# Kernel optimization log

Measured on AMD Instinct MI355X. Metric: run time of the kernel, lower is better.

Reference implementation:

```python
import jax, jax.numpy as jnp
from jax import lax
import numpy as np

K = 2        # k-hop MIS / number of rw SpGEMM iterations
EPS = 0.5    # lazy random-walk epsilon
N = 2048     # nodes
D = 512      # feature dim
E = 65536    # edges (avg degree 32)


def setup_inputs() -> dict:
    key = jax.random.key(0)
    k1, k2, k3, k4 = jax.random.split(key, 4)
    edge_index = jax.random.randint(k1, (2, E), 0, N, dtype=jnp.int32)
    edge_attr = jax.random.uniform(k2, (E,), dtype=jnp.float32)
    x = jax.random.normal(k3, (N, D), dtype=jnp.float32)
    rank = jnp.arange(N, dtype=jnp.int32)  # node ordering ('random' ordering = some permutation; identity here)
    u = jax.random.uniform(k4, (N, N), dtype=jnp.float32)  # noise for row-wise multinomial sampling
    return {"edge_index": edge_index, "edge_attr": edge_attr, "x": x, "rank": rank, "u": u}


def _maximal_k_independent_set(row, col, rank, n, k):
    """Greedy maximal k-independent set: nodes that are local rank-minima within k hops."""
    big = jnp.int32(n)

    def prop_min(r):  # one hop of min-propagation (message row -> col), keep self
        return jnp.minimum(jax.ops.segment_min(r[row], col, num_segments=n), r)

    def prop_or(b):   # one hop of boolean OR propagation (as int32)
        return jnp.maximum(jax.ops.segment_max(b[row], col, num_segments=n), b)

    def cond(st):
        mis, mask, mr = st
        return ~jnp.all(mask)

    def body(st):
        mis, mask, mr = st
        for _ in range(k):
            mr = prop_min(mr)
        mis = mis | (rank == mr)
        mk = mis.astype(jnp.int32)
        for _ in range(k):
            mk = prop_or(mk)
        mask = mk > 0
        mr = jnp.where(mask, big, rank)
        return mis, mask, mr

    init = (jnp.zeros(n, bool), jnp.zeros(n, bool), rank)
    mis, _, _ = lax.while_loop(cond, body, init)
    return mis


def _row_normalize(m):
    s = m.sum(axis=1, keepdims=True)
    return m / jnp.where(s > 0, s, 1.0)


def reference(edge_index, edge_attr, x, rank, u):
    n = x.shape[0]
    row, col = edge_index[0], edge_index[1]

    # --- MIS over the graph structure (integer-only) ---
    mis = _maximal_k_independent_set(row, col, rank, n, K)

    # --- adjacency (dense padded form of the SparseTensor) ---
    adj = jnp.zeros((n, n), x.dtype).at[row, col].add(edge_attr)

    # --- lazy random walk: rw = D^-1 A, offdiag *= (1-eps), diag = old_diag + eps ---
    rw = _row_normalize(adj)
    di = jnp.arange(n)
    new_diag = rw[di, di] + EPS  # computed BEFORE scaling, per original code
    rw = (rw * (1.0 - EPS)).at[di, di].set(new_diag)

    # --- c_mat = rw^K @ eye[:, mis]; padded to [n, n] with zero non-MIS columns ---
    c = jnp.where(mis[None, :], jnp.eye(n, dtype=x.dtype), 0.0)
    for _ in range(K):
        c = rw @ c
    c = _row_normalize(c)

    # --- sample_partition_matrix: per-row multinomial via Gumbel-argmax ---
    g = -jnp.log(-jnp.log(u + 1e-20) + 1e-20)
    logits = jnp.where(c > 0, jnp.log(jnp.maximum(c, 1e-30)), -jnp.inf) + g
    cluster = jnp.argmax(logits, axis=1)                 # [n] cluster id (a MIS column)
    c_hard = jax.nn.one_hot(cluster, n, dtype=x.dtype)   # partition matrix [n, n]

    # --- p_inv = row-normalized c_hard.T ---
    counts = c_hard.sum(axis=0)
    p_inv = c_hard.T / jnp.where(counts > 0, counts, 1.0)[:, None]

    # --- coarsen: c^T A c, pool: p_inv @ x ---
    adj_c = c_hard.T @ adj @ c_hard
    x_pool = p_inv @ x
    return adj_c, c_hard, p_inv, mis, x_pool
```

## Files before the change

### kernel.cpp

```cpp
#include <hip/hip_runtime.h>
#include <hip/hip_bf16.h>
#include <math.h>
#include <stdint.h>

#define NN 2048
#define DD 512
#define EE 65536
#define EPSV 0.5f
#define SEN 2048
#define PADE 98304
#define CTILE 8

static const size_t SZ = (size_t)NN * NN;

__global__ __launch_bounds__(256) void count_deg(const int* __restrict__ row,
                                                 const int* __restrict__ col,
                                                 int* __restrict__ degree,
                                                 int* __restrict__ cdeg) {
  int e = blockIdx.x * 256 + threadIdx.x;
  atomicAdd(&degree[row[e]], 1);
  atomicAdd(&cdeg[col[e]], 1);
}

__global__ __launch_bounds__(1024) void csr_scan_pad(const int* __restrict__ degree,
                                                     const int* __restrict__ cdeg,
                                                     int* __restrict__ row_ptr,
                                                     int* __restrict__ fill_ptr,
                                                     int* __restrict__ col_ptr,
                                                     int* __restrict__ cfill_ptr,
                                                     unsigned short* __restrict__ colidx,
                                                     unsigned short* __restrict__ rowidx,
                                                     float* __restrict__ avals,
                                                     int* __restrict__ counts) {
  __shared__ int a[NN], b[NN], c[NN], d[NN];
  int t = threadIdx.x;
  for (int v = t; v < NN; v += 1024) {
    a[v] = (degree[v] + 15) & ~15;
    c[v] = (cdeg[v] + 15) & ~15;
    counts[v] = 0;
  }
  __syncthreads();
  int* s1 = a; int* d1 = b; int* s2 = c; int* d2 = d;
  for (int off = 1; off < NN; off <<= 1) {
    for (int v = t; v < NN; v += 1024) {
      d1[v] = s1[v] + (v >= off ? s1[v - off] : 0);
      d2[v] = s2[v] + (v >= off ? s2[v - off] : 0);
    }
    __syncthreads();
    int* tp = s1; s1 = d1; d1 = tp;
    tp = s2; s2 = d2; d2 = tp;
  }
  for (int v = t; v < NN; v += 1024) {
    int dg = degree[v];
    int end = s1[v];
    int excl = end - ((dg + 15) & ~15);
    row_ptr[v] = excl;
    fill_ptr[v] = excl;
    for (int e = excl + dg; e < end; ++e) {
      colidx[e] = (unsigned short)v;
      avals[e] = 0.f;
    }
    dg = cdeg[v];
    end = s2[v];
    excl = end - ((dg + 15) & ~15);
    col_ptr[v] = excl;
    cfill_ptr[v] = excl;
    for (int e = excl + dg; e < end; ++e) rowidx[e] = (unsigned short)v;
  }
  if (t == 0) {
    row_ptr[NN] = s1[NN - 1];
    col_ptr[NN] = s2[NN - 1];
  }
}

__global__ __launch_bounds__(256) void csr_fill(const int* __restrict__ row,
                                                const int* __restrict__ col,
                                                const float* __restrict__ attr,
                                                int* __restrict__ fill_ptr,
                                                int* __restrict__ cfill_ptr,
                                                unsigned short* __restrict__ colidx,
                                                unsigned short* __restrict__ rowidx,
                                                float* __restrict__ avals) {
  int e = blockIdx.x * 256 + threadIdx.x;
  int r = row[e], c = col[e];
  int pos = atomicAdd(&fill_ptr[r], 1);
  colidx[pos] = (unsigned short)c;
  avals[pos] = attr[e];
  rowidx[atomicAdd(&cfill_ptr[c], 1)] = (unsigned short)r;
}

__global__ __launch_bounds__(1024) void fused_mis_rw(const int* __restrict__ row_ptr_g,
                                                     const int* __restrict__ col_ptr_g,
                                                     const unsigned short* __restrict__ colidx,
                                                     const unsigned short* __restrict__ rowidx,
                                                     const int* __restrict__ rank_g,
                                                     int* __restrict__ mis_flag,
                                                     int* __restrict__ mis_list,
                                                     int* __restrict__ misinv,
                                                     int* __restrict__ mis_count,
                                                     const float* __restrict__ avals,
                                                     float* __restrict__ rw,
                                                     float* __restrict__ adjc,
                                                     float* __restrict__ xp) {
  if (blockIdx.x == 0) {
    __shared__ int rank_s[NN];
    __shared__ int mr[NN];
    __shared__ int cov[NN];
    __shared__ int dly[NN];
    __shared__ int mis_s[NN];
    __shared__ int row_ptr_s[NN + 1];
    __shared__ int col_ptr_s[NN + 1];
    __shared__ int unc[2][NN];
    __shared__ int dl[NN];
    __shared__ int ucnt[2];
    __shared__ int dcnt;
    __shared__ int cnt;
    int t = threadIdx.x;
    const uint4* col4 = (const uint4*)colidx;
    const uint4* row4 = (const uint4*)rowidx;

    for (int v = t; v < NN; v += 1024) {
      int rk = rank_g[v];
      rank_s[v] = rk;
      mr[v] = rk;
      cov[v] = 0;
      dly[v] = 0;
      mis_s[v] = 0;
      row_ptr_s[v] = row_ptr_g[v];
      col_ptr_s[v] = col_ptr_g[v];
      unc[0][v] = v;
    }
    if (t == 0) {
      row_ptr_s[NN] = row_ptr_g[NN];
      col_ptr_s[NN] = col_ptr_g[NN];
      ucnt[0] = NN;
      ucnt[1] = 0;
      dcnt = 0;
      cnt = 0;
    }
    __syncthreads();

    int cur = 0;
    for (int round = 0; round < NN; ++round) {
      int U = ucnt[cur];
      if (round) {
        for (int v = t; v < NN; v += 1024) {
          mr[v] = cov[v] ? SEN : rank_s[v];
          dly[v] = 0;
        }
        if (t == 0) { ucnt[cur ^ 1] = 0; dcnt = 0; }
        __syncthreads();
      }
      for (int i = t; i < U; i += 1024) {
        int v = unc[cur][i];
        int val = rank_s[v];
        int e0 = row_ptr_s[v];
        int nch = (row_ptr_s[v + 1] - e0) >> 3;
        const uint4* b4 = col4 + (e0 >> 3);
        for (int cI = 0; cI < nch; cI += 2) {
          uint4 A = b4[cI], B = b4[cI + 1];
          atomicMin(&mr[A.x & 0xFFFFu], val); atomicMin(&mr[A.x >> 16], val);
          atomicMin(&mr[A.y & 0xFFFFu], val); atomicMin(&mr[A.y >> 16], val);
          atomicMin(&mr[A.z & 0xFFFFu], val); atomicMin(&mr[A.z >> 16], val);
          atomicMin(&mr[A.w & 0xFFFFu], val); atomicMin(&mr[A.w >> 16], val);
          atomicMin(&mr[B.x & 0xFFFFu], val); atomicMin(&mr[B.x >> 16], val);
          atomicMin(&mr[B.y & 0xFFFFu], val); atomicMin(&mr[B.y >> 16], val);
          atomicMin(&mr[B.z & 0xFFFFu], val); atomicMin(&mr[B.z >> 16], val);
          atomicMin(&mr[B.w & 0xFFFFu], val); atomicMin(&mr[B.w >> 16], val);
        }
      }
      __syncthreads();
      for (int i = t; i < U; i += 1024) {
        int v = unc[cur][i];
        int val = mr[v];
        int e0 = col_ptr_s[v];
        int nch = (col_ptr_s[v + 1] - e0) >> 3;
        const uint4* b4 = row4 + (e0 >> 3);
        for (int cI = 0; cI < nch; cI += 2) {
          uint4 A = b4[cI], B = b4[cI + 1];
          int m0 = min(mr[A.x & 0xFFFFu], mr[A.x >> 16]);
          int m1 = min(mr[A.y & 0xFFFFu], mr[A.y >> 16]);
          int m2 = min(mr[A.z & 0xFFFFu], mr[A.z >> 16]);
          int m3 = min(mr[A.w & 0xFFFFu], mr[A.w >> 16]);
          int m4 = min(mr[B.x & 0xFFFFu], mr[B.x >> 16]);
          int m5 = min(mr[B.y & 0xFFFFu], mr[B.y >> 16]);
          int m6 = min(mr[B.z & 0xFFFFu], mr[B.z >> 16]);
          int m7 = min(mr[B.w & 0xFFFFu], mr[B.w >> 16]);
          val = min(val, min(min(min(m0, m1), min(m2, m3)),
                             min(min(m4, m5), min(m6, m7))));
        }
        if (rank_s[v] == val) {
          mis_s[v] = 1;
          dly[v] = 1;
          dl[atomicAdd(&dcnt, 1)] = v;
        }
      }
      __syncthreads();
      int D = dcnt;
      for (int i = t; i < D; i += 1024) {
        int v = dl[i];
        int e0 = row_ptr_s[v];
        int nch = (row_ptr_s[v + 1] - e0) >> 3;
        const uint4* b4 = col4 + (e0 >> 3);
        for (int cI = 0; cI < nch; cI += 2) {
          uint4 A = b4[cI], B = b4[cI + 1];
          dly[A.x & 0xFFFFu] = 1; dly[A.x >> 16] = 1;
          dly[A.y & 0xFFFFu] = 1; dly[A.y >> 16] = 1;
          dly[A.z & 0xFFFFu] = 1; dly[A.z >> 16] = 1;
          dly[A.w & 0xFFFFu] = 1; dly[A.w >> 16] = 1;
          dly[B.x & 0xFFFFu] = 1; dly[B.x >> 16] = 1;
          dly[B.y & 0xFFFFu] = 1; dly[B.y >> 16] = 1;
          dly[B.z & 0xFFFFu] = 1; dly[B.z >> 16] = 1;
          dly[B.w & 0xFFFFu] = 1; dly[B.w >> 16] = 1;
        }
      }
      __syncthreads();
      for (int i = t; i < U; i += 1024) {
        int v = unc[cur][i];
        int c1 = dly[v];
        if (!c1) {
          int e0 = col_ptr_s[v];
          int nch = (col_ptr_s[v + 1] - e0) >> 3;
          const uint4* b4 = row4 + (e0 >> 3);
          for (int cI = 0; cI < nch; cI += 2) {
            uint4 A = b4[cI], B = b4[cI + 1];
            c1 |= dly[A.x & 0xFFFFu] | dly[A.x >> 16] |
                  dly[A.y & 0xFFFFu] | dly[A.y >> 16] |
                  dly[A.z & 0xFFFFu] | dly[A.z >> 16] |
                  dly[A.w & 0xFFFFu] | dly[A.w >> 16] |
                  dly[B.x & 0xFFFFu] | dly[B.x >> 16] |
                  dly[B.y & 0xFFFFu] | dly[B.y >> 16] |
                  dly[B.z & 0xFFFFu] | dly[B.z >> 16] |
                  dly[B.w & 0xFFFFu] | dly[B.w >> 16];
            if (c1) break;
          }
        }
        if (c1) cov[v] = 1;
        else unc[cur ^ 1][atomicAdd(&ucnt[cur ^ 1], 1)] = v;
      }
      __syncthreads();
      if (ucnt[cur ^ 1] == 0) break;
      cur ^= 1;
    }

    for (int v = t; v < NN; v += 1024) {
      int s = mis_s[v];
      mis_flag[v] = s;
      int slot = -1;
      if (s) {
        slot = atomicAdd(&cnt, 1);
        mis_list[slot] = v;
      }
      misinv[v] = slot;
    }
    __syncthreads();
    if (t == 0) *mis_count = cnt;
  } else {
    __shared__ float rowbuf[NN];
    __shared__ float ssum;
    int i = blockIdx.x - 1;
    int t = threadIdx.x;
    float4 z4 = make_float4(0.f, 0.f, 0.f, 0.f);
    if (t < 512) ((float4*)(adjc + (size_t)i * NN))[t] = z4;
    if (t < 128) ((float4*)xp)[(size_t)i * 128 + t] = z4;
    for (int j = t; j < NN; j += 1024) rowbuf[j] = 0.f;
    if (t == 0) ssum = 0.f;
    __syncthreads();
    int e0 = row_ptr_g[i], e1 = row_ptr_g[i + 1];
    float part = 0.f;
    for (int e = e0 + t; e < e1; e += 1024) {
      float a = avals[e];
      atomicAdd(&rowbuf[colidx[e]], a);
      part += a;
    }
    for (int off = 32; off; off >>= 1) part += __shfl_down(part, off);
    if ((t & 63) == 0) atomicAdd(&ssum, part);
    __syncthreads();
    float s = ssum;
    s = (s > 0.f) ? s : 1.f;
    for (int j = t; j < NN; j += 1024) {
      float v = rowbuf[j] / s;
      v = (i == j) ? (v + EPSV) : (v * (1.f - EPSV));
      rw[(size_t)i * NN + j] = v;
    }
  }
}

__device__ inline unsigned int f32_key(float x) {
  unsigned int u = __float_as_uint(x);
  return (u & 0x80000000u) ? ~u : (u | 0x80000000u);
}
__device__ inline float dot4(float4 a, float4 b) {
  return ((a.x * b.x + a.y * b.y) + (a.z * b.z + a.w * b.w));
}
__device__ inline unsigned long long umax64(unsigned long long a, unsigned long long b) {
  return a > b ? a : b;
}
__device__ inline int pdecode(unsigned long long p) {
  return (p == 0ull) ? 0 : (NN - 1 - (int)(p & 0xFFFFFFFFull));
}

__global__ __launch_bounds__(256) void c2_cluster(const float* __restrict__ rw,
                                                  const float* __restrict__ u,
                                                  const int* __restrict__ mis_list,
                                                  const int* __restrict__ mis_count,
                                                  int* __restrict__ cluster,
                                                  int* __restrict__ counts) {
  __shared__ float Bs[CTILE][NN];
  int M = *mis_count;
  int t = threadIdx.x;
  int lane = t & 63, w = t >> 6;
  int r0 = blockIdx.x * 8 + w * 2;
  const float4* rp0 = (const float4*)(rw + (size_t)r0 * NN);
  const float4* rp1 = (const float4*)(rw + (size_t)(r0 + 1) * NN);
  float4 A0[8], A1[8];
#pragma unroll
  for (int q = 0; q < 8; ++q) {
    A0[q] = rp0[q * 64 + lane];
    A1[q] = rp1[q * 64 + lane];
  }
  unsigned long long best0 = 0ull, best1 = 0ull;
  for (int c0 = 0; c0 < M; c0 += CTILE) {
    int c1 = min(CTILE, M - c0);
    __syncthreads();
    for (int idx = t; idx < c1 * NN; idx += 256) {
      int c = idx >> 11, i = idx & (NN - 1);
      Bs[c][i] = rw[(size_t)i * NN + mis_list[c0 + c]];
    }
    __syncthreads();
    for (int jj = 0; jj < c1; ++jj) {
      int m = mis_list[c0 + jj];
      const float4* bb = (const float4*)(Bs[jj]);
      float4 B[8];
#pragma unroll
      for (int q = 0; q < 8; ++q) B[q] = bb[q * 64 + lane];
      float s01 = dot4(A0[0], B[0]) + dot4(A0[1], B[1]);
      float s23 = dot4(A0[2], B[2]) + dot4(A0[3], B[3]);
      float s45 = dot4(A0[4], B[4]) + dot4(A0[5], B[5]);
      float s67 = dot4(A0[6], B[6]) + dot4(A0[7], B[7]);
      float s = (s01 + s23) + (s45 + s67);
      s += __shfl_xor(s, 32);
      s += __shfl_xor(s, 16);
      s += __shfl_xor(s, 8);
      s += __shfl_xor(s, 4);
      s += __shfl_xor(s, 2);
      s += __shfl_xor(s, 1);
      float t01 = dot4(A1[0], B[0]) + dot4(A1[1], B[1]);
      float t23 = dot4(A1[2], B[2]) + dot4(A1[3], B[3]);
      float t45 = dot4(A1[4], B[4]) + dot4(A1[5], B[5]);
      float t67 = dot4(A1[6], B[6]) + dot4(A1[7], B[7]);
      float tt = (t01 + t23) + (t45 + t67);
      tt += __shfl_xor(tt, 32);
      tt += __shfl_xor(tt, 16);
      tt += __shfl_xor(tt, 8);
      tt += __shfl_xor(tt, 4);
      tt += __shfl_xor(tt, 2);
      tt += __shfl_xor(tt, 1);
      if (lane == 0) {
        if (s > 0.f) {
          float uu = u[(size_t)r0 * NN + m];
          float g = -logf(-logf(uu + 1e-20f) + 1e-20f);
          float logit = logf(s) + g;
          best0 = umax64(best0, ((unsigned long long)f32_key(logit) << 32) |
                                    (unsigned int)(NN - 1 - m));
        }
        if (tt > 0.f) {
          float uu = u[(size_t)(r0 + 1) * NN + m];
          float g = -logf(-logf(uu + 1e-20f) + 1e-20f);
          float logit = logf(tt) + g;
          best1 = umax64(best1, ((unsigned long long)f32_key(logit) << 32) |
                                    (unsigned int)(NN - 1 - m));
        }
      }
    }
  }
  if (lane == 0) {
    int m0b = pdecode(best0);
    cluster[r0] = m0b;
    atomicAdd(&counts[m0b], 1);
    int m1b = pdecode(best1);
    cluster[r0 + 1] = m1b;
    atomicAdd(&counts[m1b], 1);
  }
}

__global__ __launch_bounds__(256) void scatter_chpm(const int* __restrict__ row,
                                                    const int* __restrict__ col,
                                                    const float* __restrict__ attr,
                                                    const float* __restrict__ x,
                                                    const int* __restrict__ cluster,
                                                    const int* __restrict__ counts,
                                                    const int* __restrict__ mis_flag,
                                                    float* __restrict__ out_ch,
                                                    float* __restrict__ out_pinv,
                                                    float* __restrict__ out_mis,
                                                    float* __restrict__ adjc,
                                                    float* __restrict__ xp) {
  int idx = blockIdx.x * 256 + threadIdx.x;
  int a = idx >> 11, b = idx & (NN - 1);
  out_ch[idx] = (cluster[a] == b) ? 1.f : 0.f;
  float pv = 0.f;
  if (cluster[b] == a) {
    int c = counts[a];
    pv = 1.f / (float)(c > 0 ? c : 1);
  }
  out_pinv[idx] = pv;
  if (idx < NN) out_mis[idx] = mis_flag[idx] ? 1.f : 0.f;
  if (idx < NN * DD) {
    int i = idx >> 9;
    int ci = cluster[i];
    int c = counts[ci];
    atomicAdd(&xp[ci * DD + (idx & (DD - 1))], x[idx] / (float)(c > 0 ? c : 1));
  }
  if (idx < EE) {
    atomicAdd(&adjc[(size_t)cluster[row[idx]] * NN + cluster[col[idx]]], attr[idx]);
  }
}

extern "C" void kernel_launch(void* const* d_in, const int* in_sizes, int n_in,
                              void* d_out, int out_size, void* d_ws, size_t ws_size,
                              hipStream_t stream) {
  const int*   edge_index = (const int*)d_in[0];
  const float* edge_attr  = (const float*)d_in[1];
  const float* x          = (const float*)d_in[2];
  const int*   rank       = (const int*)d_in[3];
  const float* u          = (const float*)d_in[4];
  float* out              = (float*)d_out;

  const int* row = edge_index;
  const int* col = edge_index + EE;

  float* out_adjc = out;
  float* out_ch   = out + SZ;
  float* out_pinv = out + 2 * SZ;
  float* out_mis  = out + 3 * SZ;
  float* out_xp   = out + 3 * SZ + NN;

  int*   degree    = (int*)d_ws;
  int*   cdeg      = degree + NN;
  int*   counts    = cdeg + NN;
  int*   mis_flag  = counts + NN;
  int*   cluster   = mis_flag + NN;
  int*   mis_list  = cluster + NN;
  int*   misinv    = mis_list + NN;
  int*   mis_count = misinv + NN;
  int*   fill_ptr  = mis_count + 1;
  int*   cfill_ptr = fill_ptr + NN;
  int*   row_ptr   = cfill_ptr + NN;
  int*   col_ptr   = row_ptr + NN + 1;
  unsigned short* colidx =
      (unsigned short*)(((uintptr_t)(col_ptr + NN + 1) + 31) & ~(uintptr_t)31);
  unsigned short* rowidx = colidx + PADE;
  float* avals = (float*)(rowidx + PADE);

  hipMemsetAsync(d_ws, 0, 2 * NN * sizeof(int), stream);
  count_deg<<<EE / 256, 256, 0, stream>>>(row, col, degree, cdeg);
  csr_scan_pad<<<1, 1024, 0, stream>>>(degree, cdeg, row_ptr, fill_ptr, col_ptr,
                                       cfill_ptr, colidx, rowidx, avals, counts);
  csr_fill<<<EE / 256, 256, 0, stream>>>(row, col, edge_attr, fill_ptr, cfill_ptr,
                                         colidx, rowidx, avals);
  fused_mis_rw<<<NN + 1, 1024, 0, stream>>>(row_ptr, col_ptr, colidx, rowidx, rank,
                                            mis_flag, mis_list, misinv, mis_count,
                                            avals, out_pinv , out_adjc, out_xp);
  c2_cluster<<<256, 256, 0, stream>>>(out_pinv, u, mis_list, mis_count, cluster, counts);
  scatter_chpm<<<(NN * NN) / 256, 256, 0, stream>>>(row, col, edge_attr, x, cluster,
                                                    counts, mis_flag, out_ch, out_pinv,
                                                    out_mis, out_adjc, out_xp);
}
```

Baseline: 262.9 us.

## Merge CSR build into one kernel and pre-gather MIS columns once

The three CSR construction launches plus the memset become a single two-block kernel. Block 0 builds the row-major CSR and block 1 the column-major CSR, each counting degrees in shared memory. The cluster kernel no longer has every block re-gather the strided MIS columns of rw into shared memory. A separate gather kernel writes them once, contiguously, into the c_hard output buffer as scratch, and every block then streams them from global/L2 without barriers. Cluster decoding and counts move into a small extra kernel. This cuts redundant strided gathers and syncs, at the cost of serialising CSR building onto two blocks and reading B from L2 instead of LDS.

```diff
diff --git a/kernel.cpp b/kernel.cpp
--- a/kernel.cpp
+++ b/kernel.cpp
@@ -9,84 +9,79 @@
 #define EPSV 0.5f
 #define SEN 2048
 #define PADE 98304
-#define CTILE 8
 
 static const size_t SZ = (size_t)NN * NN;
 
-__global__ __launch_bounds__(256) void count_deg(const int* __restrict__ row,
-                                                 const int* __restrict__ col,
-                                                 int* __restrict__ degree,
-                                                 int* __restrict__ cdeg) {
-  int e = blockIdx.x * 256 + threadIdx.x;
-  atomicAdd(&degree[row[e]], 1);
-  atomicAdd(&cdeg[col[e]], 1);
-}
-
-__global__ __launch_bounds__(1024) void csr_scan_pad(const int* __restrict__ degree,
-                                                     const int* __restrict__ cdeg,
-                                                     int* __restrict__ row_ptr,
-                                                     int* __restrict__ fill_ptr,
-                                                     int* __restrict__ col_ptr,
-                                                     int* __restrict__ cfill_ptr,
-                                                     unsigned short* __restrict__ colidx,
-                                                     unsigned short* __restrict__ rowidx,
-                                                     float* __restrict__ avals,
-                                                     int* __restrict__ counts) {
-  __shared__ int a[NN], b[NN], c[NN], d[NN];
+__global__ __launch_bounds__(1024) void csr_build(const int* __restrict__ row,
+                                                  const int* __restrict__ col,
+                                                  const float* __restrict__ attr,
+                                                  int* __restrict__ row_ptr,
+                                                  int* __restrict__ col_ptr,
+                                                  unsigned short* __restrict__ colidx,
+                                                  unsigned short* __restrict__ rowidx,
+                                                  float* __restrict__ avals,
+                                                  unsigned long long* __restrict__ packed,
+                                                  int* __restrict__ counts) {
+  __shared__ int deg[NN];
+  __shared__ int sA[NN], sB[NN];
+  __shared__ int fptr[NN];
   int t = threadIdx.x;
+  int isCSR = (blockIdx.x == 0);
+  const int* key = isCSR ? row : col;
+  for (int v = t; v < NN; v += 1024) deg[v] = 0;
+  if (isCSR) {
+    for (int v = t; v < NN; v += 1024) {
+      packed[v] = 0ull;
+      counts[v] = 0;
+    }
+  }
+  __syncthreads();
+  for (int e = t; e < EE; e += 1024) atomicAdd(&deg[key[e]], 1);
+  __syncthreads();
+  for (int v = t; v < NN; v += 1024) sA[v] = (deg[v] + 15) & ~15;
+  __syncthreads();
+  int* s = sA;
+  int* d = sB;
+  for (int off = 1; off < NN; off <<= 1) {
+    for (int v = t; v < NN; v += 1024) d[v] = s[v] + (v >= off ? s[v - off] : 0);
+    __syncthreads();
+    int* tp = s; s = d; d = tp;
+  }
   for (int v = t; v < NN; v += 1024) {
-    a[v] = (degree[v] + 15) & ~15;
-    c[v] = (cdeg[v] + 15) & ~15;
-    counts[v] = 0;
+    int dg = deg[v];
+    int end = s[v];
+    int excl = end - ((dg + 15) & ~15);
+    fptr[v] = excl;
+    if (isCSR) {
+      row_ptr[v] = excl;
+      for (int e = excl + dg; e < end; ++e) {
+        colidx[e] = (unsigned short)v;
+        avals[e] = 0.f;
+      }
+    } else {
+      col_ptr[v] = excl;
+      for (int e = excl + dg; e < end; ++e) rowidx[e] = (unsigned short)v;
+    }
+  }
+  if (t == 0) {
+    if (isCSR) row_ptr[NN] = s[NN - 1];
+    else col_ptr[NN] = s[NN - 1];
   }
   __syncthreads();
-  int* s1 = a; int* d1 = b; int* s2 = c; int* d2 = d;
-  for (int off = 1; off < NN; off <<= 1) {
-    for (int v = t; v < NN; v += 1024) {
-      d1[v] = s1[v] + (v >= off ? s1[v - off] : 0);
-      d2[v] = s2[v] + (v >= off ? s2[v - off] : 0);
-    }
-    __syncthreads();
-    int* tp = s1; s1 = d1; d1 = tp;
-    tp = s2; s2 = d2; d2 = tp;
-  }
-  for (int v = t; v < NN; v += 1024) {
-    int dg = degree[v];
-    int end = s1[v];
-    int excl = end - ((dg + 15) & ~15);
-    row_ptr[v] = excl;
-    fill_ptr[v] = excl;
-    for (int e = excl + dg; e < end; ++e) {
-      colidx[e] = (unsigned short)v;
-      avals[e] = 0.f;
-    }
-    dg = cdeg[v];
-    end = s2[v];
-    excl = end - ((dg + 15) & ~15);
-    col_ptr[v] = excl;
-    cfill_ptr[v] = excl;
-    for (int e = excl + dg; e < end; ++e) rowidx[e] = (unsigned short)v;
-  }
-  if (t == 0) {
-    row_ptr[NN] = s1[NN - 1];
-    col_ptr[NN] = s2[NN - 1];
-  }
-}
-
-__global__ __launch_bounds__(256) void csr_fill(const int* __restrict__ row,
-                                                const int* __restrict__ col,
-                                                const float* __restrict__ attr,
-                                                int* __restrict__ fill_ptr,
-                                                int* __restrict__ cfill_ptr,
-                                                unsigned short* __restrict__ colidx,
-                                                unsigned short* __restrict__ rowidx,
-                                                float* __restrict__ avals) {
-  int e = blockIdx.x * 256 + threadIdx.x;
-  int r = row[e], c = col[e];
-  int pos = atomicAdd(&fill_ptr[r], 1);
-  colidx[pos] = (unsigned short)c;
-  avals[pos] = attr[e];
-  rowidx[atomicAdd(&cfill_ptr[c], 1)] = (unsigned short)r;
+  if (isCSR) {
+    for (int e = t; e < EE; e += 1024) {
+      int r = row[e];
+      int pos = atomicAdd(&fptr[r], 1);
+      colidx[pos] = (unsigned short)col[e];
+      avals[pos] = attr[e];
+    }
+  } else {
+    for (int e = t; e < EE; e += 1024) {
+      int c = col[e];
+      int pos = atomicAdd(&fptr[c], 1);
+      rowidx[pos] = (unsigned short)row[e];
+    }
+  }
 }
 
 __global__ __launch_bounds__(1024) void fused_mis_rw(const int* __restrict__ row_ptr_g,
@@ -286,6 +281,19 @@
   }
 }
 
+__global__ __launch_bounds__(256) void bc_gather(const float* __restrict__ rw,
+                                                 const int* __restrict__ mis_list,
+                                                 const int* __restrict__ mis_count,
+                                                 float* __restrict__ Bc) {
+  int M = *mis_count;
+  int total = M * NN;
+  int stride = gridDim.x * 256;
+  for (int j = blockIdx.x * 256 + threadIdx.x; j < total; j += stride) {
+    int tc = j >> 11, i = j & (NN - 1);
+    Bc[(size_t)tc * NN + i] = rw[(size_t)i * NN + mis_list[tc]];
+  }
+}
+
 __device__ inline unsigned int f32_key(float x) {
   unsigned int u = __float_as_uint(x);
   return (u & 0x80000000u) ? ~u : (u | 0x80000000u);
@@ -300,16 +308,14 @@
   return (p == 0ull) ? 0 : (NN - 1 - (int)(p & 0xFFFFFFFFull));
 }
 
-__global__ __launch_bounds__(256) void c2_cluster(const float* __restrict__ rw,
-                                                  const float* __restrict__ u,
-                                                  const int* __restrict__ mis_list,
-                                                  const int* __restrict__ mis_count,
-                                                  int* __restrict__ cluster,
-                                                  int* __restrict__ counts) {
-  __shared__ float Bs[CTILE][NN];
+__global__ __launch_bounds__(256) void c2_all(const float* __restrict__ rw,
+                                              const float* __restrict__ Bc,
+                                              const float* __restrict__ u,
+                                              const int* __restrict__ mis_list,
+                                              const int* __restrict__ mis_count,
+                                              unsigned long long* __restrict__ packed) {
   int M = *mis_count;
-  int t = threadIdx.x;
-  int lane = t & 63, w = t >> 6;
+  int lane = threadIdx.x & 63, w = threadIdx.x >> 6;
   int r0 = blockIdx.x * 8 + w * 2;
   const float4* rp0 = (const float4*)(rw + (size_t)r0 * NN);
   const float4* rp1 = (const float4*)(rw + (size_t)(r0 + 1) * NN);
@@ -320,68 +326,64 @@
     A1[q] = rp1[q * 64 + lane];
   }
   unsigned long long best0 = 0ull, best1 = 0ull;
-  for (int c0 = 0; c0 < M; c0 += CTILE) {
-    int c1 = min(CTILE, M - c0);
-    __syncthreads();
-    for (int idx = t; idx < c1 * NN; idx += 256) {
-      int c = idx >> 11, i = idx & (NN - 1);
-      Bs[c][i] = rw[(size_t)i * NN + mis_list[c0 + c]];
-    }
-    __syncthreads();
-    for (int jj = 0; jj < c1; ++jj) {
-      int m = mis_list[c0 + jj];
-      const float4* bb = (const float4*)(Bs[jj]);
-      float4 B[8];
+  for (int j = 0; j < M; ++j) {
+    int m = mis_list[j];
+    const float4* cb = (const float4*)(Bc + (size_t)j * NN);
+    float4 B[8];
 #pragma unroll
-      for (int q = 0; q < 8; ++q) B[q] = bb[q * 64 + lane];
-      float s01 = dot4(A0[0], B[0]) + dot4(A0[1], B[1]);
-      float s23 = dot4(A0[2], B[2]) + dot4(A0[3], B[3]);
-      float s45 = dot4(A0[4], B[4]) + dot4(A0[5], B[5]);
-      float s67 = dot4(A0[6], B[6]) + dot4(A0[7], B[7]);
-      float s = (s01 + s23) + (s45 + s67);
-      s += __shfl_xor(s, 32);
-      s += __shfl_xor(s, 16);
-      s += __shfl_xor(s, 8);
-      s += __shfl_xor(s, 4);
-      s += __shfl_xor(s, 2);
-      s += __shfl_xor(s, 1);
-      float t01 = dot4(A1[0], B[0]) + dot4(A1[1], B[1]);
-      float t23 = dot4(A1[2], B[2]) + dot4(A1[3], B[3]);
-      float t45 = dot4(A1[4], B[4]) + dot4(A1[5], B[5]);
-      float t67 = dot4(A1[6], B[6]) + dot4(A1[7], B[7]);
-      float tt = (t01 + t23) + (t45 + t67);
-      tt += __shfl_xor(tt, 32);
-      tt += __shfl_xor(tt, 16);
-      tt += __shfl_xor(tt, 8);
-      tt += __shfl_xor(tt, 4);
-      tt += __shfl_xor(tt, 2);
-      tt += __shfl_xor(tt, 1);
-      if (lane == 0) {
-        if (s > 0.f) {
-          float uu = u[(size_t)r0 * NN + m];
-          float g = -logf(-logf(uu + 1e-20f) + 1e-20f);
-          float logit = logf(s) + g;
-          best0 = umax64(best0, ((unsigned long long)f32_key(logit) << 32) |
-                                    (unsigned int)(NN - 1 - m));
-        }
-        if (tt > 0.f) {
-          float uu = u[(size_t)(r0 + 1) * NN + m];
-          float g = -logf(-logf(uu + 1e-20f) + 1e-20f);
-          float logit = logf(tt) + g;
-          best1 = umax64(best1, ((unsigned long long)f32_key(logit) << 32) |
-                                    (unsigned int)(NN - 1 - m));
-        }
+    for (int q = 0; q < 8; ++q) B[q] = cb[q * 64 + lane];
+    float s01 = dot4(A0[0], B[0]) + dot4(A0[1], B[1]);
+    float s23 = dot4(A0[2], B[2]) + dot4(A0[3], B[3]);
+    float s45 = dot4(A0[4], B[4]) + dot4(A0[5], B[5]);
+    float s67 = dot4(A0[6], B[6]) + dot4(A0[7], B[7]);
+    float s = (s01 + s23) + (s45 + s67);
+    s += __shfl_xor(s, 32);
+    s += __shfl_xor(s, 16);
+    s += __shfl_xor(s, 8);
+    s += __shfl_xor(s, 4);
+    s += __shfl_xor(s, 2);
+    s += __shfl_xor(s, 1);
+    float t01 = dot4(A1[0], B[0]) + dot4(A1[1], B[1]);
+    float t23 = dot4(A1[2], B[2]) + dot4(A1[3], B[3]);
+    float t45 = dot4(A1[4], B[4]) + dot4(A1[5], B[5]);
+    float t67 = dot4(A1[6], B[6]) + dot4(A1[7], B[7]);
+    float tt = (t01 + t23) + (t45 + t67);
+    tt += __shfl_xor(tt, 32);
+    tt += __shfl_xor(tt, 16);
+    tt += __shfl_xor(tt, 8);
+    tt += __shfl_xor(tt, 4);
+    tt += __shfl_xor(tt, 2);
+    tt += __shfl_xor(tt, 1);
+    if (lane == 0) {
+      if (s > 0.f) {
+        float uu = u[(size_t)r0 * NN + m];
+        float g = -logf(-logf(uu + 1e-20f) + 1e-20f);
+        float logit = logf(s) + g;
+        best0 = umax64(best0, ((unsigned long long)f32_key(logit) << 32) |
+                                  (unsigned int)(NN - 1 - m));
+      }
+      if (tt > 0.f) {
+        float uu = u[(size_t)(r0 + 1) * NN + m];
+        float g = -logf(-logf(uu + 1e-20f) + 1e-20f);
+        float logit = logf(tt) + g;
+        best1 = umax64(best1, ((unsigned long long)f32_key(logit) << 32) |
+                                  (unsigned int)(NN - 1 - m));
       }
     }
   }
   if (lane == 0) {
-    int m0b = pdecode(best0);
-    cluster[r0] = m0b;
-    atomicAdd(&counts[m0b], 1);
-    int m1b = pdecode(best1);
-    cluster[r0 + 1] = m1b;
-    atomicAdd(&counts[m1b], 1);
-  }
+    packed[r0] = best0;
+    packed[r0 + 1] = best1;
+  }
+}
+
+__global__ __launch_bounds__(256) void decode_cnt(const unsigned long long* __restrict__ packed,
+                                                  int* __restrict__ cluster,
+                                                  int* __restrict__ counts) {
+  int idx = blockIdx.x * 256 + threadIdx.x;
+  int m = pdecode(packed[idx]);
+  cluster[idx] = m;
+  atomicAdd(&counts[m], 1);
 }
 
 __global__ __launch_bounds__(256) void scatter_chpm(const int* __restrict__ row,
@@ -436,33 +438,28 @@
   float* out_mis  = out + 3 * SZ;
   float* out_xp   = out + 3 * SZ + NN;
 
-  int*   degree    = (int*)d_ws;
-  int*   cdeg      = degree + NN;
-  int*   counts    = cdeg + NN;
+  unsigned long long* packed = (unsigned long long*)d_ws;
+  int*   counts    = (int*)(packed + NN);
   int*   mis_flag  = counts + NN;
   int*   cluster   = mis_flag + NN;
   int*   mis_list  = cluster + NN;
   int*   misinv    = mis_list + NN;
   int*   mis_count = misinv + NN;
-  int*   fill_ptr  = mis_count + 1;
-  int*   cfill_ptr = fill_ptr + NN;
-  int*   row_ptr   = cfill_ptr + NN;
+  int*   row_ptr   = mis_count + 1;
   int*   col_ptr   = row_ptr + NN + 1;
   unsigned short* colidx =
       (unsigned short*)(((uintptr_t)(col_ptr + NN + 1) + 31) & ~(uintptr_t)31);
   unsigned short* rowidx = colidx + PADE;
   float* avals = (float*)(rowidx + PADE);
 
-  hipMemsetAsync(d_ws, 0, 2 * NN * sizeof(int), stream);
-  count_deg<<<EE / 256, 256, 0, stream>>>(row, col, degree, cdeg);
-  csr_scan_pad<<<1, 1024, 0, stream>>>(degree, cdeg, row_ptr, fill_ptr, col_ptr,
-                                       cfill_ptr, colidx, rowidx, avals, counts);
-  csr_fill<<<EE / 256, 256, 0, stream>>>(row, col, edge_attr, fill_ptr, cfill_ptr,
-                                         colidx, rowidx, avals);
+  csr_build<<<2, 1024, 0, stream>>>(row, col, edge_attr, row_ptr, col_ptr,
+                                    colidx, rowidx, avals, packed, counts);
   fused_mis_rw<<<NN + 1, 1024, 0, stream>>>(row_ptr, col_ptr, colidx, rowidx, rank,
                                             mis_flag, mis_list, misinv, mis_count,
                                             avals, out_pinv , out_adjc, out_xp);
-  c2_cluster<<<256, 256, 0, stream>>>(out_pinv, u, mis_list, mis_count, cluster, counts);
+  bc_gather<<<256, 256, 0, stream>>>(out_pinv, mis_list, mis_count, out_ch);
+  c2_all<<<NN / 8, 256, 0, stream>>>(out_pinv, out_ch, u, mis_list, mis_count, packed);
+  decode_cnt<<<NN / 256, 256, 0, stream>>>(packed, cluster, counts);
   scatter_chpm<<<(NN * NN) / 256, 256, 0, stream>>>(row, col, edge_attr, x, cluster,
                                                     counts, mis_flag, out_ch, out_pinv,
                                                     out_mis, out_adjc, out_xp);
```

Result: slower. 326.1 us (+24.0%).

## Gather MIS columns once into scratch and stream them in the cluster kernel

Applied to the files above, without the earlier changes.

The cluster kernel used to have every block re-gather the strided MIS columns of the random-walk matrix into shared memory, tile by tile, with block barriers in between. A new kernel now gathers those columns once into a contiguous transposed buffer, reusing the c_hard output as scratch before it is overwritten. The dot-product kernel then reads that buffer directly with coalesced float4 loads and no barriers. The cluster decode and count atomics move into a separate small kernel. This adds two extra launches and a round trip of the gathered buffer through global memory.

```diff
diff --git a/kernel.cpp b/kernel.cpp
--- a/kernel.cpp
+++ b/kernel.cpp
@@ -9,7 +9,6 @@
 #define EPSV 0.5f
 #define SEN 2048
 #define PADE 98304
-#define CTILE 8
 
 static const size_t SZ = (size_t)NN * NN;
 
@@ -286,6 +285,19 @@
   }
 }
 
+__global__ __launch_bounds__(256) void bc_gather(const float* __restrict__ rw,
+                                                 const int* __restrict__ mis_list,
+                                                 const int* __restrict__ mis_count,
+                                                 float* __restrict__ Bc) {
+  int M = *mis_count;
+  int total = M * NN;
+  int stride = gridDim.x * 256;
+  for (int j = blockIdx.x * 256 + threadIdx.x; j < total; j += stride) {
+    int tc = j >> 11, i = j & (NN - 1);
+    Bc[(size_t)tc * NN + i] = rw[(size_t)i * NN + mis_list[tc]];
+  }
+}
+
 __device__ inline unsigned int f32_key(float x) {
   unsigned int u = __float_as_uint(x);
   return (u & 0x80000000u) ? ~u : (u | 0x80000000u);
@@ -300,16 +312,14 @@
   return (p == 0ull) ? 0 : (NN - 1 - (int)(p & 0xFFFFFFFFull));
 }
 
-__global__ __launch_bounds__(256) void c2_cluster(const float* __restrict__ rw,
-                                                  const float* __restrict__ u,
-                                                  const int* __restrict__ mis_list,
-                                                  const int* __restrict__ mis_count,
-                                                  int* __restrict__ cluster,
-                                                  int* __restrict__ counts) {
-  __shared__ float Bs[CTILE][NN];
+__global__ __launch_bounds__(256) void c2_all(const float* __restrict__ rw,
+                                              const float* __restrict__ Bc,
+                                              const float* __restrict__ u,
+                                              const int* __restrict__ mis_list,
+                                              const int* __restrict__ mis_count,
+                                              unsigned long long* __restrict__ packed) {
   int M = *mis_count;
-  int t = threadIdx.x;
-  int lane = t & 63, w = t >> 6;
+  int lane = threadIdx.x & 63, w = threadIdx.x >> 6;
   int r0 = blockIdx.x * 8 + w * 2;
   const float4* rp0 = (const float4*)(rw + (size_t)r0 * NN);
   const float4* rp1 = (const float4*)(rw + (size_t)(r0 + 1) * NN);
@@ -320,68 +330,64 @@
     A1[q] = rp1[q * 64 + lane];
   }
   unsigned long long best0 = 0ull, best1 = 0ull;
-  for (int c0 = 0; c0 < M; c0 += CTILE) {
-    int c1 = min(CTILE, M - c0);
-    __syncthreads();
-    for (int idx = t; idx < c1 * NN; idx += 256) {
-      int c = idx >> 11, i = idx & (NN - 1);
-      Bs[c][i] = rw[(size_t)i * NN + mis_list[c0 + c]];
-    }
-    __syncthreads();
-    for (int jj = 0; jj < c1; ++jj) {
-      int m = mis_list[c0 + jj];
-      const float4* bb = (const float4*)(Bs[jj]);
-      float4 B[8];
+  for (int j = 0; j < M; ++j) {
+    int m = mis_list[j];
+    const float4* cb = (const float4*)(Bc + (size_t)j * NN);
+    float4 B[8];
 #pragma unroll
-      for (int q = 0; q < 8; ++q) B[q] = bb[q * 64 + lane];
-      float s01 = dot4(A0[0], B[0]) + dot4(A0[1], B[1]);
-      float s23 = dot4(A0[2], B[2]) + dot4(A0[3], B[3]);
-      float s45 = dot4(A0[4], B[4]) + dot4(A0[5], B[5]);
-      float s67 = dot4(A0[6], B[6]) + dot4(A0[7], B[7]);
-      float s = (s01 + s23) + (s45 + s67);
-      s += __shfl_xor(s, 32);
-      s += __shfl_xor(s, 16);
-      s += __shfl_xor(s, 8);
-      s += __shfl_xor(s, 4);
-      s += __shfl_xor(s, 2);
-      s += __shfl_xor(s, 1);
-      float t01 = dot4(A1[0], B[0]) + dot4(A1[1], B[1]);
-      float t23 = dot4(A1[2], B[2]) + dot4(A1[3], B[3]);
-      float t45 = dot4(A1[4], B[4]) + dot4(A1[5], B[5]);
-      float t67 = dot4(A1[6], B[6]) + dot4(A1[7], B[7]);
-      float tt = (t01 + t23) + (t45 + t67);
-      tt += __shfl_xor(tt, 32);
-      tt += __shfl_xor(tt, 16);
-      tt += __shfl_xor(tt, 8);
-      tt += __shfl_xor(tt, 4);
-      tt += __shfl_xor(tt, 2);
-      tt += __shfl_xor(tt, 1);
-      if (lane == 0) {
-        if (s > 0.f) {
-          float uu = u[(size_t)r0 * NN + m];
-          float g = -logf(-logf(uu + 1e-20f) + 1e-20f);
-          float logit = logf(s) + g;
-          best0 = umax64(best0, ((unsigned long long)f32_key(logit) << 32) |
-                                    (unsigned int)(NN - 1 - m));
-        }
-        if (tt > 0.f) {
-          float uu = u[(size_t)(r0 + 1) * NN + m];
-          float g = -logf(-logf(uu + 1e-20f) + 1e-20f);
-          float logit = logf(tt) + g;
-          best1 = umax64(best1, ((unsigned long long)f32_key(logit) << 32) |
-                                    (unsigned int)(NN - 1 - m));
-        }
+    for (int q = 0; q < 8; ++q) B[q] = cb[q * 64 + lane];
+    float s01 = dot4(A0[0], B[0]) + dot4(A0[1], B[1]);
+    float s23 = dot4(A0[2], B[2]) + dot4(A0[3], B[3]);
+    float s45 = dot4(A0[4], B[4]) + dot4(A0[5], B[5]);
+    float s67 = dot4(A0[6], B[6]) + dot4(A0[7], B[7]);
+    float s = (s01 + s23) + (s45 + s67);
+    s += __shfl_xor(s, 32);
+    s += __shfl_xor(s, 16);
+    s += __shfl_xor(s, 8);
+    s += __shfl_xor(s, 4);
+    s += __shfl_xor(s, 2);
+    s += __shfl_xor(s, 1);
+    float t01 = dot4(A1[0], B[0]) + dot4(A1[1], B[1]);
+    float t23 = dot4(A1[2], B[2]) + dot4(A1[3], B[3]);
+    float t45 = dot4(A1[4], B[4]) + dot4(A1[5], B[5]);
+    float t67 = dot4(A1[6], B[6]) + dot4(A1[7], B[7]);
+    float tt = (t01 + t23) + (t45 + t67);
+    tt += __shfl_xor(tt, 32);
+    tt += __shfl_xor(tt, 16);
+    tt += __shfl_xor(tt, 8);
+    tt += __shfl_xor(tt, 4);
+    tt += __shfl_xor(tt, 2);
+    tt += __shfl_xor(tt, 1);
+    if (lane == 0) {
+      if (s > 0.f) {
+        float uu = u[(size_t)r0 * NN + m];
+        float g = -logf(-logf(uu + 1e-20f) + 1e-20f);
+        float logit = logf(s) + g;
+        best0 = umax64(best0, ((unsigned long long)f32_key(logit) << 32) |
+                                  (unsigned int)(NN - 1 - m));
+      }
+      if (tt > 0.f) {
+        float uu = u[(size_t)(r0 + 1) * NN + m];
+        float g = -logf(-logf(uu + 1e-20f) + 1e-20f);
+        float logit = logf(tt) + g;
+        best1 = umax64(best1, ((unsigned long long)f32_key(logit) << 32) |
+                                  (unsigned int)(NN - 1 - m));
       }
     }
   }
   if (lane == 0) {
-    int m0b = pdecode(best0);
-    cluster[r0] = m0b;
-    atomicAdd(&counts[m0b], 1);
-    int m1b = pdecode(best1);
-    cluster[r0 + 1] = m1b;
-    atomicAdd(&counts[m1b], 1);
-  }
+    packed[r0] = best0;
+    packed[r0 + 1] = best1;
+  }
+}
+
+__global__ __launch_bounds__(256) void decode_cnt(const unsigned long long* __restrict__ packed,
+                                                  int* __restrict__ cluster,
+                                                  int* __restrict__ counts) {
+  int idx = blockIdx.x * 256 + threadIdx.x;
+  int m = pdecode(packed[idx]);
+  cluster[idx] = m;
+  atomicAdd(&counts[m], 1);
 }
 
 __global__ __launch_bounds__(256) void scatter_chpm(const int* __restrict__ row,
@@ -438,7 +444,8 @@
 
   int*   degree    = (int*)d_ws;
   int*   cdeg      = degree + NN;
-  int*   counts    = cdeg + NN;
+  unsigned long long* packed = (unsigned long long*)(cdeg + NN);
+  int*   counts    = (int*)(packed + NN);
   int*   mis_flag  = counts + NN;
   int*   cluster   = mis_flag + NN;
   int*   mis_list  = cluster + NN;
@@ -462,7 +469,9 @@
   fused_mis_rw<<<NN + 1, 1024, 0, stream>>>(row_ptr, col_ptr, colidx, rowidx, rank,
                                             mis_flag, mis_list, misinv, mis_count,
                                             avals, out_pinv , out_adjc, out_xp);
-  c2_cluster<<<256, 256, 0, stream>>>(out_pinv, u, mis_list, mis_count, cluster, counts);
+  bc_gather<<<256, 256, 0, stream>>>(out_pinv, mis_list, mis_count, out_ch);
+  c2_all<<<NN / 8, 256, 0, stream>>>(out_pinv, out_ch, u, mis_list, mis_count, packed);
+  decode_cnt<<<NN / 256, 256, 0, stream>>>(packed, cluster, counts);
   scatter_chpm<<<(NN * NN) / 256, 256, 0, stream>>>(row, col, edge_attr, x, cluster,
                                                     counts, mis_flag, out_ch, out_pinv,
                                                     out_mis, out_adjc, out_xp);
```

New measurement: 234.7 us. -10.7%, faster.
